# Kernel tuning notes

Hardware: AMD Instinct MI355X
Metric: run time of the kernel (lower is better)

The kernel has to match this reference:

```python
import jax, jax.numpy as jnp
import numpy as np

HID = 512
NB = 20
N = 65536
EPS = 1e-5


def layer_norm(x, g, b):
    m = jnp.mean(x, axis=-1, keepdims=True)
    v = jnp.mean(jnp.square(x - m), axis=-1, keepdims=True)
    return (x - m) * jax.lax.rsqrt(v + EPS) * g + b


def setup_inputs() -> dict:
    key = jax.random.key(0)
    ks = jax.random.split(key, 8)
    s = 0.02
    return {
        "x": jax.random.normal(ks[0], (N, 2), dtype=jnp.float32),
        "in_w": jax.random.normal(ks[1], (2, HID), dtype=jnp.float32) * s,
        "in_b": jnp.zeros((HID,), jnp.float32),
        "ln1_g": jnp.ones((NB, HID), jnp.float32),
        "ln1_b": jnp.zeros((NB, HID), jnp.float32),
        "fc1_w": jax.random.normal(ks[2], (NB, HID, HID), dtype=jnp.float32) * s,
        "fc1_b": jnp.zeros((NB, HID), jnp.float32),
        "ln2_g": jnp.ones((NB, HID), jnp.float32),
        "ln2_b": jnp.zeros((NB, HID), jnp.float32),
        "fc2_w": jax.random.normal(ks[3], (NB, HID, HID), dtype=jnp.float32) * s,
        "fc2_b": jnp.zeros((NB, HID), jnp.float32),
        "out_ln_g": jnp.ones((HID,), jnp.float32),
        "out_ln_b": jnp.zeros((HID,), jnp.float32),
        "out_w": jax.random.normal(ks[4], (HID, 1), dtype=jnp.float32) * s,
        "out_b": jnp.zeros((1,), jnp.float32),
    }


def reference(x, in_w, in_b, ln1_g, ln1_b, fc1_w, fc1_b, ln2_g, ln2_b,
              fc2_w, fc2_b, out_ln_g, out_ln_b, out_w, out_b):
    # in_proj + SiLU: [N,2] @ [2,HID]
    h = jax.nn.silu(x @ in_w + in_b)

    def block(h, p):
        g1, b1, w1, c1, g2, b2, w2, c2 = p
        t = jax.nn.silu(layer_norm(h, g1, b1) @ w1 + c1)
        t = layer_norm(t, g2, b2) @ w2 + c2
        return h + t, None

    h, _ = jax.lax.scan(block, h, (ln1_g, ln1_b, fc1_w, fc1_b,
                                   ln2_g, ln2_b, fc2_w, fc2_b))
    h = jax.nn.silu(layer_norm(h, out_ln_g, out_ln_b))
    return h @ out_w + out_b  # [N, 1]
```

## Files before the change

### kernel.cpp

```cpp
#include <hip/hip_runtime.h>
#include <hip/hip_bf16.h>


typedef float  fvec4 __attribute__((ext_vector_type(4)));
typedef __bf16 bvec8 __attribute__((ext_vector_type(8)));

#define HN_STRIDE 520
#define WCHUNK    32768
#define SMEM_BYTES (64*HN_STRIDE*2 + 64*8)
#define WPK_USHORTS ((size_t)20*2*8*WCHUNK)

__device__ __forceinline__ unsigned int f2bf(float v) {
    unsigned int u = __float_as_uint(v);
    return (u + 0x7fffu + ((u >> 16) & 1u)) >> 16;
}
__device__ __forceinline__ unsigned int pkbf(float a, float b) {
    __hip_bfloat162 t = __float22bfloat162_rn(make_float2(a, b));
    unsigned int r;
    __builtin_memcpy(&r, &t, 4);
    return r;
}
__device__ __forceinline__ float silu_f(float v) {
    return v * (1.0f / (1.0f + __expf(-v)));
}

__global__ __launch_bounds__(256) void pack_weights(
        const float* __restrict__ w1, const float* __restrict__ w2,
        const float* __restrict__ g1, const float* __restrict__ g2,
        unsigned short* __restrict__ pk) {
    int tid = blockIdx.x * 256 + threadIdx.x;
    int l  = tid & 63;
    int f  = tid >> 6;
    int t  = f & 3;
    int kc = (f >> 2) & 15;
    int w  = (f >> 6) & 7;
    int g  = (f >> 9) & 1;
    int b  = f >> 10;
    const float* src = g ? w2 : w1;
    const float* gs  = (g ? g2 : g1) + b * 512;
    int k0 = kc * 32 + (l >> 4) * 8;
    int n  = w * 64 + (l & 15) * 4 + t;
    const float* s = src + ((size_t)b * 512 + k0) * 512 + n;
    unsigned int r[4];
#pragma unroll
    for (int j = 0; j < 4; ++j) {
        float ga = gs[k0 + 2 * j];
        float gb = gs[k0 + 2 * j + 1];
        unsigned int lo = f2bf(ga * s[(size_t)(2*j) * 512]);
        unsigned int hi = f2bf(gb * s[(size_t)(2*j + 1) * 512]);
        r[j] = lo | (hi << 16);
    }
    *(uint4*)(pk + (size_t)tid * 8) = make_uint4(r[0], r[1], r[2], r[3]);
}

__global__ __launch_bounds__(512) void make_uv(
        const float* __restrict__ w1, const float* __restrict__ w2,
        const float* __restrict__ g1, const float* __restrict__ bl1,
        const float* __restrict__ cb1,
        const float* __restrict__ g2, const float* __restrict__ bl2,
        const float* __restrict__ cb2,
        float* __restrict__ uv) {
    int b = blockIdx.x >> 1, slot = blockIdx.x & 1, n = threadIdx.x;
    const float* W  = (slot ? w2 : w1) + (size_t)b * 512 * 512;
    const float* g  = (slot ? g2 : g1) + b * 512;
    const float* bl = (slot ? bl2 : bl1) + b * 512;
    const float* cb = (slot ? cb2 : cb1) + b * 512;
    float u = 0.f, v = 0.f;
    for (int j = 0; j < 512; ++j) {
        float wv = W[(size_t)j * 512 + n];
        u = fmaf(g[j], wv, u);
        v = fmaf(bl[j], wv, v);
    }
    uv[((b * 2 + slot) * 2 + 0) * 512 + n] = u;
    uv[((b * 2 + slot) * 2 + 1) * 512 + n] = v + cb[n];
}

__device__ __forceinline__ void acc_u32(unsigned int u, float& s, float& ss) {
    float lo = __uint_as_float(u << 16);
    float hi = __uint_as_float(u & 0xFFFF0000u);
    s += lo + hi;
    ss = __builtin_fmaf(lo, lo, ss);
    ss = __builtin_fmaf(hi, hi, ss);
}

__device__ __forceinline__ void gemm_red(
        fvec4 acc[4][4], const unsigned short* hn,
        const unsigned short* __restrict__ wp, const uint4* pre,
        float2* mv, int l, int c, int q, int tid, int rot) {
    const uint4* wp4 = (const uint4*)wp;
    const int r = tid >> 3, j = tid & 7;
    float s = 0.f, ss = 0.f;
    uint4 bcur[4] = {pre[0], pre[1], pre[2], pre[3]};
#pragma unroll
    for (int it = 0; it < 16; ++it) {
        const int kc = (it + rot) & 15;
        uint4 bnxt[4];
        if (it < 15) {
            const int kn = (kc + 1) & 15;
#pragma unroll
            for (int t = 0; t < 4; ++t) bnxt[t] = wp4[(kn * 4 + t) * 64 + l];
        }
        bvec8 a[4];
#pragma unroll
        for (int rb = 0; rb < 4; ++rb)
            a[rb] = *(const bvec8*)(hn + (rb * 16 + c) * HN_STRIDE + kc * 32 + q * 8);
        if (it >= 4 && it < 12) {
            uint4 pv = *(const uint4*)(hn + r * HN_STRIDE + (j + 8 * (it - 4)) * 8);
            acc_u32(pv.x, s, ss); acc_u32(pv.y, s, ss);
            acc_u32(pv.z, s, ss); acc_u32(pv.w, s, ss);
        }
#pragma unroll
        for (int rb = 0; rb < 4; ++rb) {
#pragma unroll
            for (int t = 0; t < 4; ++t) {
                bvec8 bb;
                __builtin_memcpy(&bb, &bcur[t], 16);
                acc[rb][t] = __builtin_amdgcn_mfma_f32_16x16x32_bf16(a[rb], bb, acc[rb][t], 0, 0, 0);
            }
        }
        if (it < 15) {
#pragma unroll
            for (int t = 0; t < 4; ++t) bcur[t] = bnxt[t];
        }
    }
    s += __shfl_xor(s, 1); ss += __shfl_xor(ss, 1);
    s += __shfl_xor(s, 2); ss += __shfl_xor(ss, 2);
    s += __shfl_xor(s, 4); ss += __shfl_xor(ss, 4);
    if (j == 0) {
        float mean = s * (1.f / 512.f);
        float var  = ss * (1.f / 512.f) - mean * mean;
        mv[r] = make_float2(mean, rsqrtf(var + 1e-5f));
    }
}

__device__ __forceinline__ void reduce_mv_hn(const unsigned short* hn,
                                             float2* mv, int tid) {
    int r = tid >> 3, j = tid & 7;
    float s = 0.f, ss = 0.f;
#pragma unroll
    for (int u = 0; u < 8; ++u) {
        uint4 pv = *(const uint4*)(hn + r * HN_STRIDE + (j + 8 * u) * 8);
        acc_u32(pv.x, s, ss); acc_u32(pv.y, s, ss);
        acc_u32(pv.z, s, ss); acc_u32(pv.w, s, ss);
    }
    s += __shfl_xor(s, 1); ss += __shfl_xor(ss, 1);
    s += __shfl_xor(s, 2); ss += __shfl_xor(ss, 2);
    s += __shfl_xor(s, 4); ss += __shfl_xor(ss, 4);
    if (j == 0) {
        float mean = s * (1.f / 512.f);
        float var  = ss * (1.f / 512.f) - mean * mean;
        mv[r] = make_float2(mean, rsqrtf(var + 1e-5f));
    }
}

__global__ __launch_bounds__(512, 2) void mlp_fused(
        const float* __restrict__ x,
        const float* __restrict__ in_w,  const float* __restrict__ in_b,
        const float* __restrict__ out_ln_g, const float* __restrict__ out_ln_b,
        const float* __restrict__ out_w, const float* __restrict__ out_b,
        const unsigned short* __restrict__ wpk,
        const float* __restrict__ uv,
        float* __restrict__ out) {
    extern __shared__ char smem[];
    unsigned short* hn = (unsigned short*)smem;
    float* hnf = (float*)smem;
    float2* mv = (float2*)(smem + 64 * HN_STRIDE * 2);

    const int tid = threadIdx.x;
    const int w = tid >> 6;
    const int l = tid & 63, c = l & 15, q = l >> 4;
    const int colbase = w * 64 + c * 4;
    const int row0 = blockIdx.x * 64;
    const int rot = blockIdx.x & 15;

    float h[4][4][4];

    {
        fvec4 iw0 = *(const fvec4*)(in_w + colbase);
        fvec4 iw1 = *(const fvec4*)(in_w + 512 + colbase);
        fvec4 ib  = *(const fvec4*)(in_b + colbase);
#pragma unroll
        for (int rb = 0; rb < 4; ++rb)
#pragma unroll
            for (int i = 0; i < 4; ++i) {
                int row = rb * 16 + q * 4 + i;
                float2 xv = *(const float2*)(x + (size_t)(row0 + row) * 2);
#pragma unroll
                for (int t = 0; t < 4; ++t)
                    h[rb][i][t] = silu_f(xv.x * iw0[t] + xv.y * iw1[t] + ib[t]);
                *(uint2*)(hn + row * HN_STRIDE + colbase) =
                    make_uint2(pkbf(h[rb][i][0], h[rb][i][1]),
                               pkbf(h[rb][i][2], h[rb][i][3]));
            }
    }

    for (int b = 0; b < 20; ++b) {
        const unsigned short* wp1 = wpk + (size_t)(b * 16 + w) * WCHUNK;
        const unsigned short* wp2 = wpk + (size_t)(b * 16 + 8 + w) * WCHUNK;
        fvec4 u1  = *(const fvec4*)(uv + ((b * 2 + 0) * 2 + 0) * 512 + colbase);
        fvec4 vc1 = *(const fvec4*)(uv + ((b * 2 + 0) * 2 + 1) * 512 + colbase);
        fvec4 u2  = *(const fvec4*)(uv + ((b * 2 + 1) * 2 + 0) * 512 + colbase);
        fvec4 vc2 = *(const fvec4*)(uv + ((b * 2 + 1) * 2 + 1) * 512 + colbase);

        uint4 pre[4];
#pragma unroll
        for (int t = 0; t < 4; ++t)
            pre[t] = ((const uint4*)wp1)[(rot * 4 + t) * 64 + l];
        __syncthreads();

        fvec4 acc[4][4];
#pragma unroll
        for (int rb = 0; rb < 4; ++rb)
#pragma unroll
            for (int t = 0; t < 4; ++t) acc[rb][t] = (fvec4){0.f, 0.f, 0.f, 0.f};
        gemm_red(acc, hn, wp1, pre, mv, l, c, q, tid, rot);
        __syncthreads();

#pragma unroll
        for (int t = 0; t < 4; ++t)
            pre[t] = ((const uint4*)wp2)[(rot * 4 + t) * 64 + l];
#pragma unroll
        for (int rb = 0; rb < 4; ++rb)
#pragma unroll
            for (int i = 0; i < 4; ++i) {
                int row = rb * 16 + q * 4 + i;
                float2 m = mv[row];
                float inv = m.y, minv = -m.x * m.y;
                float t0 = silu_f(__builtin_fmaf(acc[rb][0][i], inv,
                                  __builtin_fmaf(minv, u1[0], vc1[0])));
                float t1 = silu_f(__builtin_fmaf(acc[rb][1][i], inv,
                                  __builtin_fmaf(minv, u1[1], vc1[1])));
                float t2 = silu_f(__builtin_fmaf(acc[rb][2][i], inv,
                                  __builtin_fmaf(minv, u1[2], vc1[2])));
                float t3 = silu_f(__builtin_fmaf(acc[rb][3][i], inv,
                                  __builtin_fmaf(minv, u1[3], vc1[3])));
                *(uint2*)(hn + row * HN_STRIDE + colbase) =
                    make_uint2(pkbf(t0, t1), pkbf(t2, t3));
            }
        __syncthreads();

#pragma unroll
        for (int rb = 0; rb < 4; ++rb)
#pragma unroll
            for (int t = 0; t < 4; ++t) acc[rb][t] = (fvec4){0.f, 0.f, 0.f, 0.f};
        gemm_red(acc, hn, wp2, pre, mv, l, c, q, tid, rot);
        __syncthreads();

#pragma unroll
        for (int rb = 0; rb < 4; ++rb)
#pragma unroll
            for (int i = 0; i < 4; ++i) {
                int row = rb * 16 + q * 4 + i;
                float2 m = mv[row];
                float inv = m.y, minv = -m.x * m.y;
#pragma unroll
                for (int t = 0; t < 4; ++t)
                    h[rb][i][t] = __builtin_fmaf(acc[rb][t][i], inv,
                        h[rb][i][t] + __builtin_fmaf(minv, u2[t], vc2[t]));
                *(uint2*)(hn + row * HN_STRIDE + colbase) =
                    make_uint2(pkbf(h[rb][i][0], h[rb][i][1]),
                               pkbf(h[rb][i][2], h[rb][i][3]));
            }
    }

    __syncthreads();
    reduce_mv_hn(hn, mv, tid);
    __syncthreads();
    {
        fvec4 og = *(const fvec4*)(out_ln_g + colbase);
        fvec4 ob = *(const fvec4*)(out_ln_b + colbase);
        fvec4 ow = *(const fvec4*)(out_w + colbase);
        const int pcol = w * 16 + c;
#pragma unroll
        for (int rb = 0; rb < 4; ++rb)
#pragma unroll
            for (int i = 0; i < 4; ++i) {
                int row = rb * 16 + q * 4 + i;
                float2 m = mv[row];
                float sacc = 0.f;
#pragma unroll
                for (int t = 0; t < 4; ++t) {
                    float v = (h[rb][i][t] - m.x) * m.y * og[t] + ob[t];
                    sacc += silu_f(v) * ow[t];
                }
                hnf[pcol * 65 + row] = sacc;
            }
    }
    __syncthreads();
    {
        int r = tid >> 3, j = tid & 7;
        float s = 0.f;
#pragma unroll
        for (int u = 0; u < 16; ++u)
            s += hnf[(j + 8 * u) * 65 + r];
        s += __shfl_xor(s, 1);
        s += __shfl_xor(s, 2);
        s += __shfl_xor(s, 4);
        if (j == 0) out[row0 + r] = s + out_b[0];
    }
}

extern "C" void kernel_launch(void* const* d_in, const int* in_sizes, int n_in,
                              void* d_out, int out_size, void* d_ws, size_t ws_size,
                              hipStream_t stream) {
    const float* x        = (const float*)d_in[0];
    const float* in_w     = (const float*)d_in[1];
    const float* in_b     = (const float*)d_in[2];
    const float* ln1_g    = (const float*)d_in[3];
    const float* ln1_b    = (const float*)d_in[4];
    const float* fc1_w    = (const float*)d_in[5];
    const float* fc1_b    = (const float*)d_in[6];
    const float* ln2_g    = (const float*)d_in[7];
    const float* ln2_b    = (const float*)d_in[8];
    const float* fc2_w    = (const float*)d_in[9];
    const float* fc2_b    = (const float*)d_in[10];
    const float* out_ln_g = (const float*)d_in[11];
    const float* out_ln_b = (const float*)d_in[12];
    const float* out_w    = (const float*)d_in[13];
    const float* out_b    = (const float*)d_in[14];
    float* out = (float*)d_out;
    unsigned short* wpk = (unsigned short*)d_ws;
    float* uv = (float*)((char*)d_ws + WPK_USHORTS * 2);

    (void)hipFuncSetAttribute((const void*)mlp_fused,
                              hipFuncAttributeMaxDynamicSharedMemorySize, SMEM_BYTES);

    pack_weights<<<5120, 256, 0, stream>>>(fc1_w, fc2_w, ln1_g, ln2_g, wpk);
    make_uv<<<40, 512, 0, stream>>>(fc1_w, fc2_w, ln1_g, ln1_b, fc1_b,
                                    ln2_g, ln2_b, fc2_b, uv);
    mlp_fused<<<1024, 512, SMEM_BYTES, stream>>>(
        x, in_w, in_b, out_ln_g, out_ln_b, out_w, out_b, wpk, uv, out);
}
```

Before: 1.992 ms.

## Split each block's rows across two wave groups using 1024-thread blocks

Doubles the block to 16 waves, so each wave computes a 32-row by 64-column tile instead of 64 by 64. This halves the accumulator and residual registers per thread and raises the number of waves in flight. The rotated K start and the register double-buffered weight prefetch are removed, and the bf16 write-back of the residual moves to the top of each block iteration. In exchange, each weight fragment is reused across fewer rows, which doubles weight reads per block. The aggressive launch bounds may also force register spills.

After: 2.067 ms. 1.04x slower.

```diff
diff --git a/kernel.cpp b/kernel.cpp
--- a/kernel.cpp
+++ b/kernel.cpp
@@ -84,48 +84,45 @@
 }
 
 __device__ __forceinline__ void gemm_red(
-        fvec4 acc[4][4], const unsigned short* hn,
+        fvec4 acc[2][4], const unsigned short* hn,
         const unsigned short* __restrict__ wp, const uint4* pre,
-        float2* mv, int l, int c, int q, int tid, int rot) {
+        float2* mv, int l, int c, int q, int tid, int rbase) {
     const uint4* wp4 = (const uint4*)wp;
-    const int r = tid >> 3, j = tid & 7;
+    const int r = tid >> 4, j = tid & 15;
     float s = 0.f, ss = 0.f;
-    uint4 bcur[4] = {pre[0], pre[1], pre[2], pre[3]};
-#pragma unroll
-    for (int it = 0; it < 16; ++it) {
-        const int kc = (it + rot) & 15;
-        uint4 bnxt[4];
-        if (it < 15) {
-            const int kn = (kc + 1) & 15;
-#pragma unroll
-            for (int t = 0; t < 4; ++t) bnxt[t] = wp4[(kn * 4 + t) * 64 + l];
+#pragma unroll
+    for (int kc = 0; kc < 16; ++kc) {
+        bvec8 a[2];
+        uint4 br[4];
+#pragma unroll
+        for (int rb = 0; rb < 2; ++rb)
+            a[rb] = *(const bvec8*)(hn + (rbase + rb * 16 + c) * HN_STRIDE + kc * 32 + q * 8);
+        if (kc == 0) {
+#pragma unroll
+            for (int t = 0; t < 4; ++t) br[t] = pre[t];
+        } else {
+#pragma unroll
+            for (int t = 0; t < 4; ++t) br[t] = wp4[(kc * 4 + t) * 64 + l];
         }
-        bvec8 a[4];
-#pragma unroll
-        for (int rb = 0; rb < 4; ++rb)
-            a[rb] = *(const bvec8*)(hn + (rb * 16 + c) * HN_STRIDE + kc * 32 + q * 8);
-        if (it >= 4 && it < 12) {
-            uint4 pv = *(const uint4*)(hn + r * HN_STRIDE + (j + 8 * (it - 4)) * 8);
+        if (kc >= 4 && kc < 8) {
+            uint4 pv = *(const uint4*)(hn + r * HN_STRIDE + (j + 16 * (kc - 4)) * 8);
             acc_u32(pv.x, s, ss); acc_u32(pv.y, s, ss);
             acc_u32(pv.z, s, ss); acc_u32(pv.w, s, ss);
         }
 #pragma unroll
-        for (int rb = 0; rb < 4; ++rb) {
+        for (int rb = 0; rb < 2; ++rb) {
 #pragma unroll
             for (int t = 0; t < 4; ++t) {
                 bvec8 bb;
-                __builtin_memcpy(&bb, &bcur[t], 16);
+                __builtin_memcpy(&bb, &br[t], 16);
                 acc[rb][t] = __builtin_amdgcn_mfma_f32_16x16x32_bf16(a[rb], bb, acc[rb][t], 0, 0, 0);
             }
-        }
-        if (it < 15) {
-#pragma unroll
-            for (int t = 0; t < 4; ++t) bcur[t] = bnxt[t];
         }
     }
     s += __shfl_xor(s, 1); ss += __shfl_xor(ss, 1);
     s += __shfl_xor(s, 2); ss += __shfl_xor(ss, 2);
     s += __shfl_xor(s, 4); ss += __shfl_xor(ss, 4);
+    s += __shfl_xor(s, 8); ss += __shfl_xor(ss, 8);
     if (j == 0) {
         float mean = s * (1.f / 512.f);
         float var  = ss * (1.f / 512.f) - mean * mean;
@@ -135,17 +132,18 @@
 
 __device__ __forceinline__ void reduce_mv_hn(const unsigned short* hn,
                                              float2* mv, int tid) {
-    int r = tid >> 3, j = tid & 7;
+    int r = tid >> 4, j = tid & 15;
     float s = 0.f, ss = 0.f;
 #pragma unroll
-    for (int u = 0; u < 8; ++u) {
-        uint4 pv = *(const uint4*)(hn + r * HN_STRIDE + (j + 8 * u) * 8);
+    for (int u = 0; u < 4; ++u) {
+        uint4 pv = *(const uint4*)(hn + r * HN_STRIDE + (j + 16 * u) * 8);
         acc_u32(pv.x, s, ss); acc_u32(pv.y, s, ss);
         acc_u32(pv.z, s, ss); acc_u32(pv.w, s, ss);
     }
     s += __shfl_xor(s, 1); ss += __shfl_xor(ss, 1);
     s += __shfl_xor(s, 2); ss += __shfl_xor(ss, 2);
     s += __shfl_xor(s, 4); ss += __shfl_xor(ss, 4);
+    s += __shfl_xor(s, 8); ss += __shfl_xor(ss, 8);
     if (j == 0) {
         float mean = s * (1.f / 512.f);
         float var  = ss * (1.f / 512.f) - mean * mean;
@@ -153,7 +151,7 @@
     }
 }
 
-__global__ __launch_bounds__(512, 2) void mlp_fused(
+__global__ __launch_bounds__(1024, 4) void mlp_fused(
         const float* __restrict__ x,
         const float* __restrict__ in_w,  const float* __restrict__ in_b,
         const float* __restrict__ out_ln_g, const float* __restrict__ out_ln_b,
@@ -167,36 +165,35 @@
     float2* mv = (float2*)(smem + 64 * HN_STRIDE * 2);
 
     const int tid = threadIdx.x;
-    const int w = tid >> 6;
+    const int w  = tid >> 6;
+    const int rh = w >> 3;
+    const int cg = w & 7;
     const int l = tid & 63, c = l & 15, q = l >> 4;
-    const int colbase = w * 64 + c * 4;
+    const int colbase = cg * 64 + c * 4;
+    const int rbase = rh * 32;
     const int row0 = blockIdx.x * 64;
-    const int rot = blockIdx.x & 15;
-
-    float h[4][4][4];
+
+    float h[2][4][4];
 
     {
         fvec4 iw0 = *(const fvec4*)(in_w + colbase);
         fvec4 iw1 = *(const fvec4*)(in_w + 512 + colbase);
         fvec4 ib  = *(const fvec4*)(in_b + colbase);
 #pragma unroll
-        for (int rb = 0; rb < 4; ++rb)
-#pragma unroll
-            for (int i = 0; i < 4; ++i) {
-                int row = rb * 16 + q * 4 + i;
+        for (int rb = 0; rb < 2; ++rb)
+#pragma unroll
+            for (int i = 0; i < 4; ++i) {
+                int row = rbase + rb * 16 + q * 4 + i;
                 float2 xv = *(const float2*)(x + (size_t)(row0 + row) * 2);
 #pragma unroll
                 for (int t = 0; t < 4; ++t)
                     h[rb][i][t] = silu_f(xv.x * iw0[t] + xv.y * iw1[t] + ib[t]);
-                *(uint2*)(hn + row * HN_STRIDE + colbase) =
-                    make_uint2(pkbf(h[rb][i][0], h[rb][i][1]),
-                               pkbf(h[rb][i][2], h[rb][i][3]));
             }
     }
 
     for (int b = 0; b < 20; ++b) {
-        const unsigned short* wp1 = wpk + (size_t)(b * 16 + w) * WCHUNK;
-        const unsigned short* wp2 = wpk + (size_t)(b * 16 + 8 + w) * WCHUNK;
+        const unsigned short* wp1 = wpk + (size_t)(b * 16 + cg) * WCHUNK;
+        const unsigned short* wp2 = wpk + (size_t)(b * 16 + 8 + cg) * WCHUNK;
         fvec4 u1  = *(const fvec4*)(uv + ((b * 2 + 0) * 2 + 0) * 512 + colbase);
         fvec4 vc1 = *(const fvec4*)(uv + ((b * 2 + 0) * 2 + 1) * 512 + colbase);
         fvec4 u2  = *(const fvec4*)(uv + ((b * 2 + 1) * 2 + 0) * 512 + colbase);
@@ -204,26 +201,33 @@
 
         uint4 pre[4];
 #pragma unroll
-        for (int t = 0; t < 4; ++t)
-            pre[t] = ((const uint4*)wp1)[(rot * 4 + t) * 64 + l];
+        for (int t = 0; t < 4; ++t) pre[t] = ((const uint4*)wp1)[t * 64 + l];
+#pragma unroll
+        for (int rb = 0; rb < 2; ++rb)
+#pragma unroll
+            for (int i = 0; i < 4; ++i) {
+                int row = rbase + rb * 16 + q * 4 + i;
+                *(uint2*)(hn + row * HN_STRIDE + colbase) =
+                    make_uint2(pkbf(h[rb][i][0], h[rb][i][1]),
+                               pkbf(h[rb][i][2], h[rb][i][3]));
+            }
         __syncthreads();
 
-        fvec4 acc[4][4];
-#pragma unroll
-        for (int rb = 0; rb < 4; ++rb)
+        fvec4 acc[2][4];
+#pragma unroll
+        for (int rb = 0; rb < 2; ++rb)
 #pragma unroll
             for (int t = 0; t < 4; ++t) acc[rb][t] = (fvec4){0.f, 0.f, 0.f, 0.f};
-        gemm_red(acc, hn, wp1, pre, mv, l, c, q, tid, rot);
+        gemm_red(acc, hn, wp1, pre, mv, l, c, q, tid, rbase);
         __syncthreads();
 
 #pragma unroll
-        for (int t = 0; t < 4; ++t)
-            pre[t] = ((const uint4*)wp2)[(rot * 4 + t) * 64 + l];
-#pragma unroll
-        for (int rb = 0; rb < 4; ++rb)
-#pragma unroll
-            for (int i = 0; i < 4; ++i) {
-                int row = rb * 16 + q * 4 + i;
+        for (int t = 0; t < 4; ++t) pre[t] = ((const uint4*)wp2)[t * 64 + l];
+#pragma unroll
+        for (int rb = 0; rb < 2; ++rb)
+#pragma unroll
+            for (int i = 0; i < 4; ++i) {
+                int row = rbase + rb * 16 + q * 4 + i;
                 float2 m = mv[row];
                 float inv = m.y, minv = -m.x * m.y;
                 float t0 = silu_f(__builtin_fmaf(acc[rb][0][i], inv,
@@ -240,29 +244,35 @@
         __syncthreads();
 
 #pragma unroll
-        for (int rb = 0; rb < 4; ++rb)
+        for (int rb = 0; rb < 2; ++rb)
 #pragma unroll
             for (int t = 0; t < 4; ++t) acc[rb][t] = (fvec4){0.f, 0.f, 0.f, 0.f};
-        gemm_red(acc, hn, wp2, pre, mv, l, c, q, tid, rot);
+        gemm_red(acc, hn, wp2, pre, mv, l, c, q, tid, rbase);
         __syncthreads();
 
 #pragma unroll
-        for (int rb = 0; rb < 4; ++rb)
-#pragma unroll
-            for (int i = 0; i < 4; ++i) {
-                int row = rb * 16 + q * 4 + i;
+        for (int rb = 0; rb < 2; ++rb)
+#pragma unroll
+            for (int i = 0; i < 4; ++i) {
+                int row = rbase + rb * 16 + q * 4 + i;
                 float2 m = mv[row];
                 float inv = m.y, minv = -m.x * m.y;
 #pragma unroll
                 for (int t = 0; t < 4; ++t)
                     h[rb][i][t] = __builtin_fmaf(acc[rb][t][i], inv,
                         h[rb][i][t] + __builtin_fmaf(minv, u2[t], vc2[t]));
-                *(uint2*)(hn + row * HN_STRIDE + colbase) =
-                    make_uint2(pkbf(h[rb][i][0], h[rb][i][1]),
-                               pkbf(h[rb][i][2], h[rb][i][3]));
-            }
-    }
-
+            }
+    }
+
+#pragma unroll
+    for (int rb = 0; rb < 2; ++rb)
+#pragma unroll
+        for (int i = 0; i < 4; ++i) {
+            int row = rbase + rb * 16 + q * 4 + i;
+            *(uint2*)(hn + row * HN_STRIDE + colbase) =
+                make_uint2(pkbf(h[rb][i][0], h[rb][i][1]),
+                           pkbf(h[rb][i][2], h[rb][i][3]));
+        }
     __syncthreads();
     reduce_mv_hn(hn, mv, tid);
     __syncthreads();
@@ -270,12 +280,12 @@
         fvec4 og = *(const fvec4*)(out_ln_g + colbase);
         fvec4 ob = *(const fvec4*)(out_ln_b + colbase);
         fvec4 ow = *(const fvec4*)(out_w + colbase);
-        const int pcol = w * 16 + c;
-#pragma unroll
-        for (int rb = 0; rb < 4; ++rb)
-#pragma unroll
-            for (int i = 0; i < 4; ++i) {
-                int row = rb * 16 + q * 4 + i;
+        const int scol = cg * 16 + c;
+#pragma unroll
+        for (int rb = 0; rb < 2; ++rb)
+#pragma unroll
+            for (int i = 0; i < 4; ++i) {
+                int row = rbase + rb * 16 + q * 4 + i;
                 float2 m = mv[row];
                 float sacc = 0.f;
 #pragma unroll
@@ -283,19 +293,20 @@
                     float v = (h[rb][i][t] - m.x) * m.y * og[t] + ob[t];
                     sacc += silu_f(v) * ow[t];
                 }
-                hnf[pcol * 65 + row] = sacc;
+                hnf[scol * 65 + row] = sacc;
             }
     }
     __syncthreads();
     {
-        int r = tid >> 3, j = tid & 7;
+        int r = tid >> 4, j = tid & 15;
         float s = 0.f;
 #pragma unroll
-        for (int u = 0; u < 16; ++u)
-            s += hnf[(j + 8 * u) * 65 + r];
+        for (int u = 0; u < 8; ++u)
+            s += hnf[(j + 16 * u) * 65 + r];
         s += __shfl_xor(s, 1);
         s += __shfl_xor(s, 2);
         s += __shfl_xor(s, 4);
+        s += __shfl_xor(s, 8);
         if (j == 0) out[row0 + r] = s + out_b[0];
     }
 }
@@ -328,6 +339,6 @@
     pack_weights<<<5120, 256, 0, stream>>>(fc1_w, fc2_w, ln1_g, ln2_g, wpk);
     make_uv<<<40, 512, 0, stream>>>(fc1_w, fc2_w, ln1_g, ln1_b, fc1_b,
                                     ln2_g, ln2_b, fc2_b, uv);
-    mlp_fused<<<1024, 512, SMEM_BYTES, stream>>>(
+    mlp_fused<<<1024, 1024, SMEM_BYTES, stream>>>(
         x, in_w, in_b, out_ln_g, out_ln_b, out_w, out_b, wpk, uv, out);
 }
```
